# Kernel optimization log

Measured on AMD Instinct MI355X. Metric: run time of the kernel, lower is better.

The kernel has to match this reference:

```python
import jax, jax.numpy as jnp
import numpy as np

N = 512      # nodes
F_IN = 16    # raw node features; adjacency channels = 2*F_IN = 32
H = 64       # hidden
HF = 64      # hidden_final
C = 10       # num_classes
L = 3        # num_layers
E = 16384    # edges (avg degree 32)
EPS = 1e-5


def setup_inputs() -> dict:
    key = jax.random.key(0)
    ks = iter(jax.random.split(key, 40))
    rn = lambda shape, s=0.05: jax.random.normal(next(ks), shape, jnp.float32) * s
    inp = {
        'x': jax.random.normal(next(ks), (N, F_IN), jnp.float32),
        'edge_index': jax.random.randint(next(ks), (2, E), 0, N),
        # no_prop FeatureExtractor
        'np1_w': rn((HF, 2 * F_IN)), 'np1_b': rn((HF,)),
        'np2_w': rn((HF, 2 * F_IN)), 'np3_w': rn((HF, HF)),
        # first PowerfulLayer (in = 2*F_IN)
        'c0_m1_w': rn((H, 2 * F_IN)), 'c0_m1_b': rn((H,)),
        'c0_m2_w': rn((H, 2 * F_IN)), 'c0_m2_b': rn((H,)),
        'c0_m4_w': rn((H, 2 * F_IN + H)), 'c0_m4_b': rn((H,)),
        # remaining L-1 PowerfulLayers (stacked)
        'cm1_w': rn((L - 1, H, H)), 'cm1_b': rn((L - 1, H)),
        'cm2_w': rn((L - 1, H, H)), 'cm2_b': rn((L - 1, H)),
        'cm4_w': rn((L - 1, H, 2 * H)), 'cm4_b': rn((L - 1, H)),
        # batchnorms (training-mode stats; affine params)
        'bn_g': jnp.ones((L, H), jnp.float32), 'bn_b': jnp.zeros((L, H), jnp.float32),
        # per-layer FeatureExtractors (stacked)
        'fe1_w': rn((L, HF, H)), 'fe1_b': rn((L, HF)),
        'fe2_w': rn((L, HF, H)), 'fe3_w': rn((L, HF, HF)),
        # after_conv and final linear
        'ac_w': rn((HF, HF)), 'ac_b': rn((HF,)),
        'fl_w': rn((C, HF)), 'fl_b': rn((C,)),
    }
    return inp


def _lin(x, w, b=None):
    y = x @ w.T
    return y if b is None else y + b


def _extractor(u, w1, b1, w2, w3):
    # u: [B, N, N, F]; graph_class=True, aggr='add'
    n = u.shape[1]
    trace = jnp.einsum('biif->bf', u)                     # sum of diagonal entries
    out1 = _lin(trace / n, w1, b1)
    s = (u.sum(axis=(1, 2)) - trace) / (n * (n - 1))      # off-diagonal mean-ish
    out = out1 + _lin(s, w2)
    return out + _lin(jax.nn.relu(out), w3)


def _powerful(u, m1w, m1b, m2w, m2b, m4w, m4b):
    # UnitMLP with 1 layer == 1x1 conv == per-position linear (no ReLU)
    o1 = jnp.einsum('bijc,oc->bijo', u, m1w) + m1b        # [B,N,N,H]
    o2 = jnp.einsum('bijc,oc->bijo', u, m2w) + m2b
    mult = jnp.einsum('bikh,bkjh->bijh', o1, o2)          # per-channel NxN matmul
    return _lin(jnp.concatenate([mult, u], axis=-1), m4w, m4b)


def _batchnorm(u, g, b):
    # BatchNorm2d in training mode: stats over (batch, N, N) per channel, biased var
    mean = u.mean(axis=(0, 1, 2))
    var = u.var(axis=(0, 1, 2))
    return (u - mean) * jax.lax.rsqrt(var + EPS) * g + b


def reference(x, edge_index, np1_w, np1_b, np2_w, np3_w,
              c0_m1_w, c0_m1_b, c0_m2_w, c0_m2_b, c0_m4_w, c0_m4_b,
              cm1_w, cm1_b, cm2_w, cm2_b, cm4_w, cm4_b,
              bn_g, bn_b, fe1_w, fe1_b, fe2_w, fe3_w,
              ac_w, ac_b, fl_w, fl_b):
    n = x.shape[0]
    src, dst = edge_index[0], edge_index[1]
    edge_attr = jnp.concatenate([x[src], x[dst]], axis=-1)          # [E, 2F]
    A = jnp.zeros((n, n, edge_attr.shape[-1]), x.dtype).at[src, dst].add(edge_attr)
    u = A[None]                                                      # [1,N,N,2F]

    out = _extractor(u, np1_w, np1_b, np2_w, np3_w)
    nlayers = bn_g.shape[0]
    for l in range(nlayers):
        if l == 0:
            u = _powerful(u, c0_m1_w, c0_m1_b, c0_m2_w, c0_m2_b, c0_m4_w, c0_m4_b)
        else:
            u = _powerful(u, cm1_w[l - 1], cm1_b[l - 1], cm2_w[l - 1], cm2_b[l - 1],
                          cm4_w[l - 1], cm4_b[l - 1])
        u = _batchnorm(u, bn_g[l], bn_b[l])
        out = out + _extractor(u, fe1_w[l], fe1_b[l], fe2_w[l], fe3_w[l])

    out = jax.nn.relu(out) / nlayers
    out = out + jax.nn.relu(_lin(out, ac_w, ac_b))   # layer_after_conv
    # dropout with p=0.0 / eval mode is identity
    out = _lin(out, fl_w, fl_b)
    return jax.nn.log_softmax(out, axis=-1)          # [1, num_classes]
```

## Files before the change

### kernel.cpp

```cpp
#include <hip/hip_runtime.h>
#include <hip/hip_bf16.h>

#define Nn   512
#define NN   262144
#define EDG  16384

typedef unsigned short u16;
typedef short v8s __attribute__((ext_vector_type(8)));
typedef float v4f __attribute__((ext_vector_type(4)));
typedef u16 u16x8 __attribute__((ext_vector_type(8)));

__device__ __forceinline__ float b2f(u16 u) {
    union { unsigned int i; float f; } v; v.i = ((unsigned int)u) << 16; return v.f;
}
__device__ __forceinline__ u16 f2b(float f) {
    union { float f; unsigned int i; } v; v.f = f;
    unsigned int r = (v.i + 0x7FFFu + ((v.i >> 16) & 1u)) >> 16;
    return (u16)r;
}

__global__ void sentinel_kernel(float* __restrict__ out, float val) {
    if (threadIdx.x < 10) out[threadIdx.x] = val;
}

__global__ void cvt_weights(const float* __restrict__ s0, const float* __restrict__ s1,
                            const float* __restrict__ s2, const float* __restrict__ s3,
                            const float* __restrict__ s4, const float* __restrict__ s5,
                            u16* __restrict__ dst) {
    int t = blockIdx.x * 256 + threadIdx.x;
    if (t >= 43008) return;
    float v;
    if      (t < 2048)  v = s0[t];
    else if (t < 4096)  v = s1[t - 2048];
    else if (t < 10240) v = s2[t - 4096];
    else if (t < 18432) v = s3[t - 10240];
    else if (t < 26624) v = s4[t - 18432];
    else                v = s5[t - 26624];
    dst[t] = f2b(v);
}

__global__ void scatter_edges(const float* __restrict__ x, const int* __restrict__ ei,
                              float* __restrict__ A) {
    int t = blockIdx.x * 256 + threadIdx.x;
    if (t >= EDG * 32) return;
    int e = t >> 5, c = t & 31;
    int s = ei[e], d = ei[EDG + e];
    float v = (c < 16) ? x[s * 16 + c] : x[d * 16 + (c - 16)];
    atomicAdd(A + ((size_t)s * Nn + d) * 32 + c, v);
}

__global__ __launch_bounds__(256) void finalize_u0(const float* __restrict__ A,
                                                   u16* __restrict__ u0,
                                                   float* __restrict__ total) {
    __shared__ u16 L[32 * 258];
    __shared__ float red[4][32];
    int t = threadIdx.x;
    int p0 = blockIdx.x * 256;
    const float* Ar = A + (size_t)(p0 + t) * 32;
    float v[32];
#pragma unroll
    for (int c = 0; c < 32; ++c) v[c] = Ar[c];
#pragma unroll
    for (int c = 0; c < 32; ++c) L[c * 258 + t] = f2b(v[c]);
    int wv = t >> 6;
#pragma unroll
    for (int c = 0; c < 32; ++c) {
        float r = v[c];
        for (int off = 32; off > 0; off >>= 1) r += __shfl_down(r, off);
        if ((t & 63) == 0) red[wv][c] = r;
    }
    __syncthreads();
    if (t < 32) atomicAdd(total + t, red[0][t] + red[1][t] + red[2][t] + red[3][t]);
    int off = (t & 31) * 8, rb = t >> 5;
#pragma unroll
    for (int pass = 0; pass < 4; ++pass) {
        int c = pass * 8 + rb;
        u16x8 w = *(const u16x8*)(L + c * 258 + off);
        *(u16x8*)(u0 + (size_t)c * NN + p0 + off) = w;
    }
}

__global__ void trace_raw_cm(const u16* __restrict__ ucm, float* __restrict__ trraw) {
    int c = blockIdx.x, t = threadIdx.x;
    const u16* base = ucm + (size_t)c * NN;
    float s = b2f(base[(size_t)(2 * t) * 513]) + b2f(base[(size_t)(2 * t + 1) * 513]);
    for (int off = 32; off > 0; off >>= 1) s += __shfl_down(s, off);
    __shared__ float r[4];
    if ((t & 63) == 0) r[t >> 6] = s;
    __syncthreads();
    if (t == 0) trraw[c] = r[0] + r[1] + r[2] + r[3];
}

template<int NCH>
__global__ __launch_bounds__(256) void conv12_t(
    const u16* __restrict__ src,
    const float* __restrict__ sc, const float* __restrict__ sh,
    const u16* __restrict__ w1, const float* __restrict__ b1,
    const u16* __restrict__ w2, const float* __restrict__ b2,
    u16* __restrict__ dst1, u16* __restrict__ dst2)
{
    __shared__ u16 LS[8320];
    const int C = NCH * 32;
    const int t = threadIdx.x;
    const int P0 = blockIdx.x * 128;
    const int lane = t & 63, wave = t >> 6;
    const int l15 = lane & 15, quad = lane >> 4;
    const int pw = wave * 32;
    const int sr = t >> 4;
    const int so = (t & 15) * 8;

    u16x8 pf[NCH][2];
#pragma unroll
    for (int kc = 0; kc < NCH; ++kc)
#pragma unroll
        for (int ps = 0; ps < 2; ++ps)
            pf[kc][ps] = *(const u16x8*)(src + (size_t)(kc * 32 + ps * 16 + sr) * NN + P0 + so);

    v4f acc[2][4][2];
#pragma unroll
    for (int s = 0; s < 2; ++s)
#pragma unroll
        for (int mt = 0; mt < 4; ++mt)
#pragma unroll
            for (int nt = 0; nt < 2; ++nt) acc[s][mt][nt] = (v4f){0.f, 0.f, 0.f, 0.f};

    {
        u16* Ln = LS;
#pragma unroll
        for (int ps = 0; ps < 2; ++ps) {
            int c = ps * 16 + sr;
            u16x8 v = pf[0][ps];
            if (sc) {
                float s = sc[c], f = sh[c];
#pragma unroll
                for (int j = 0; j < 8; ++j) v[j] = f2b(b2f(v[j]) * s + f);
            }
            *(u16x8*)(Ln + c * 130 + so) = v;
        }
    }
    __syncthreads();
#pragma unroll
    for (int kc = 0; kc < NCH; ++kc) {
        if (kc + 1 < NCH) {
            u16* Ln = LS + ((kc + 1) & 1) * 4160;
#pragma unroll
            for (int ps = 0; ps < 2; ++ps) {
                int c = ps * 16 + sr;
                int cg = (kc + 1) * 32 + c;
                u16x8 v = pf[kc + 1][ps];
                if (sc) {
                    float s = sc[cg], f = sh[cg];
#pragma unroll
                    for (int j = 0; j < 8; ++j) v[j] = f2b(b2f(v[j]) * s + f);
                }
                *(u16x8*)(Ln + c * 130 + so) = v;
            }
        }
        v8s af1[4], af2[4];
#pragma unroll
        for (int mt = 0; mt < 4; ++mt) {
            af1[mt] = *(const v8s*)(w1 + (mt * 16 + l15) * C + kc * 32 + quad * 8);
            af2[mt] = *(const v8s*)(w2 + (mt * 16 + l15) * C + kc * 32 + quad * 8);
        }
        const u16* Lb = LS + (kc & 1) * 4160;
#pragma unroll
        for (int nt = 0; nt < 2; ++nt) {
            const int p = pw + nt * 16 + l15;
            v8s b;
#pragma unroll
            for (int j = 0; j < 8; ++j) b[j] = (short)Lb[(quad * 8 + j) * 130 + p];
#pragma unroll
            for (int mt = 0; mt < 4; ++mt) {
                acc[0][mt][nt] = __builtin_amdgcn_mfma_f32_16x16x32_bf16(af1[mt], b, acc[0][mt][nt], 0, 0, 0);
                acc[1][mt][nt] = __builtin_amdgcn_mfma_f32_16x16x32_bf16(af2[mt], b, acc[1][mt][nt], 0, 0, 0);
            }
        }
        if (kc + 1 < NCH) __syncthreads();
    }
#pragma unroll
    for (int s = 0; s < 2; ++s) {
        __syncthreads();
        const float* bb = s ? b2 : b1;
#pragma unroll
        for (int mt = 0; mt < 4; ++mt)
#pragma unroll
            for (int r = 0; r < 4; ++r) {
                const int h = mt * 16 + quad * 4 + r;
                const float bv = bb[h];
#pragma unroll
                for (int nt = 0; nt < 2; ++nt)
                    LS[h * 130 + pw + nt * 16 + l15] = f2b(acc[s][mt][nt][r] + bv);
            }
        __syncthreads();
        u16* dd = s ? dst2 : dst1;
#pragma unroll
        for (int ps = 0; ps < 4; ++ps) {
            int h = ps * 16 + sr;
            u16x8 v = *(const u16x8*)(LS + h * 130 + so);
            __builtin_nontemporal_store(v, (u16x8*)(dd + (size_t)h * NN + P0 + so));
        }
    }
}

template<int NCH>
__global__ __launch_bounds__(256) void conv4_t(
    const u16* __restrict__ mult, const u16* __restrict__ u,
    const float* __restrict__ sc, const float* __restrict__ sh,
    const u16* __restrict__ w, const float* __restrict__ bias,
    u16* __restrict__ dst,
    float* __restrict__ psum, float* __restrict__ psq, float* __restrict__ ptr)
{
    __shared__ u16 LS[8320];
    __shared__ float R1[64][4], R2[64][4];
    const int K = NCH * 32;
    const int t = threadIdx.x;
    const int P0 = blockIdx.x * 128;
    const int lane = t & 63, wave = t >> 6;
    const int l15 = lane & 15, quad = lane >> 4;
    const int pw = wave * 32;
    const int sr = t >> 4;
    const int so = (t & 15) * 8;

    u16x8 pf[NCH][2];
#pragma unroll
    for (int kc = 0; kc < NCH; ++kc)
#pragma unroll
        for (int ps = 0; ps < 2; ++ps) {
            int cg = kc * 32 + ps * 16 + sr;
            const u16* gp = (cg < 64) ? (mult + (size_t)cg * NN + P0 + so)
                                      : (u + (size_t)(cg - 64) * NN + P0 + so);
            pf[kc][ps] = *(const u16x8*)gp;
        }

    v4f acc[4][2];
#pragma unroll
    for (int mt = 0; mt < 4; ++mt)
#pragma unroll
        for (int nt = 0; nt < 2; ++nt) acc[mt][nt] = (v4f){0.f, 0.f, 0.f, 0.f};

#pragma unroll
    for (int ps = 0; ps < 2; ++ps)
        *(u16x8*)(LS + (ps * 16 + sr) * 130 + so) = pf[0][ps];
    __syncthreads();
#pragma unroll
    for (int kc = 0; kc < NCH; ++kc) {
        if (kc + 1 < NCH) {
            u16* Ln = LS + ((kc + 1) & 1) * 4160;
#pragma unroll
            for (int ps = 0; ps < 2; ++ps) {
                int c = ps * 16 + sr;
                int cg = (kc + 1) * 32 + c;
                u16x8 v = pf[kc + 1][ps];
                if (cg >= 64 && sc) {
                    float s = sc[cg - 64], f = sh[cg - 64];
#pragma unroll
                    for (int j = 0; j < 8; ++j) v[j] = f2b(b2f(v[j]) * s + f);
                }
                *(u16x8*)(Ln + c * 130 + so) = v;
            }
        }
        v8s af[4];
#pragma unroll
        for (int mt = 0; mt < 4; ++mt)
            af[mt] = *(const v8s*)(w + (mt * 16 + l15) * K + kc * 32 + quad * 8);
        const u16* Lb = LS + (kc & 1) * 4160;
#pragma unroll
        for (int nt = 0; nt < 2; ++nt) {
            const int p = pw + nt * 16 + l15;
            v8s b;
#pragma unroll
            for (int j = 0; j < 8; ++j) b[j] = (short)Lb[(quad * 8 + j) * 130 + p];
#pragma unroll
            for (int mt = 0; mt < 4; ++mt)
                acc[mt][nt] = __builtin_amdgcn_mfma_f32_16x16x32_bf16(af[mt], b, acc[mt][nt], 0, 0, 0);
        }
        if (kc + 1 < NCH) __syncthreads();
    }
    __syncthreads();
#pragma unroll
    for (int mt = 0; mt < 4; ++mt)
#pragma unroll
        for (int r = 0; r < 4; ++r) {
            const int h = mt * 16 + quad * 4 + r;
            const float bv = bias[h];
#pragma unroll
            for (int nt = 0; nt < 2; ++nt)
                LS[h * 130 + pw + nt * 16 + l15] = f2b(acc[mt][nt][r] + bv);
        }
    __syncthreads();
    {
        int c = t >> 2, q = t & 3;
        const u16* row = LS + c * 130 + q * 32;
        float s = 0.f, s2 = 0.f;
#pragma unroll
        for (int i = 0; i < 32; ++i) { float v = b2f(row[i]); s += v; s2 += v * v; }
        R1[c][q] = s; R2[c][q] = s2;
    }
    __syncthreads();
    {
        int i = P0 >> 9, j0 = P0 & 511;
        int blk = blockIdx.x;
        if (t < 64) {
            psum[t * 2048 + blk] = R1[t][0] + R1[t][1] + R1[t][2] + R1[t][3];
            psq[t * 2048 + blk]  = R2[t][0] + R2[t][1] + R2[t][2] + R2[t][3];
            if (j0 <= i && i < j0 + 128) ptr[t * 512 + i] = b2f(LS[t * 130 + (i - j0)]);
        }
    }
#pragma unroll
    for (int ps = 0; ps < 4; ++ps) {
        int h = ps * 16 + sr;
        u16x8 v = *(const u16x8*)(LS + h * 130 + so);
        __builtin_nontemporal_store(v, (u16x8*)(dst + (size_t)h * NN + P0 + so));
    }
}

__global__ __launch_bounds__(256) void bmm_mfma(const u16* __restrict__ Aall,
                                                const u16* __restrict__ Ball,
                                                u16* __restrict__ Call) {
    __shared__ u16 LA[128 * 72];
    __shared__ u16 LB[64 * 130];
    const int h = blockIdx.y;
    const int tx = blockIdx.x & 3, ty = blockIdx.x >> 2;
    const int t = threadIdx.x;
    const int lane = t & 63, wave = t >> 6;
    const int l15 = lane & 15, quad = lane >> 4;
    const int jb = wave * 32;
    const u16* Ap = Aall + (size_t)h * NN + (size_t)ty * 128 * 512;
    const u16* Bp = Ball + (size_t)h * NN + tx * 128;

    const int srow = t >> 3;
    const int scol = (t & 7) * 8;
    const int bkr = t >> 4;
    const int bjg = (t & 15) * 8;

    v4f acc[8][2];
#pragma unroll
    for (int mt = 0; mt < 8; ++mt)
#pragma unroll
        for (int nt = 0; nt < 2; ++nt) acc[mt][nt] = (v4f){0.f, 0.f, 0.f, 0.f};

    v8s ra[4], rb[4];
#pragma unroll
    for (int i = 0; i < 4; ++i) {
        ra[i] = *(const v8s*)(Ap + (size_t)(i * 32 + srow) * 512 + scol);
        rb[i] = *(const v8s*)(Bp + (size_t)(i * 16 + bkr) * 512 + bjg);
    }

    for (int ck = 0; ck < 8; ++ck) {
#pragma unroll
        for (int i = 0; i < 4; ++i) {
            *(v8s*)(LA + (i * 32 + srow) * 72 + scol) = ra[i];
            *(v8s*)(LB + (i * 16 + bkr) * 130 + bjg) = rb[i];
        }
        __syncthreads();
        if (ck < 7) {
            const int k0 = (ck + 1) * 64;
#pragma unroll
            for (int i = 0; i < 4; ++i) {
                ra[i] = *(const v8s*)(Ap + (size_t)(i * 32 + srow) * 512 + k0 + scol);
                rb[i] = *(const v8s*)(Bp + (size_t)(k0 + i * 16 + bkr) * 512 + bjg);
            }
        }
#pragma unroll
        for (int kk = 0; kk < 2; ++kk) {
            v8s b[2];
#pragma unroll
            for (int nt = 0; nt < 2; ++nt) {
                const int j = jb + nt * 16 + l15;
#pragma unroll
                for (int jj = 0; jj < 8; ++jj)
                    b[nt][jj] = (short)LB[(kk * 32 + quad * 8 + jj) * 130 + j];
            }
#pragma unroll
            for (int mh = 0; mh < 2; ++mh) {
                v8s a[4];
#pragma unroll
                for (int m = 0; m < 4; ++m)
                    a[m] = *(const v8s*)(LA + ((mh * 4 + m) * 16 + l15) * 72 + kk * 32 + quad * 8);
#pragma unroll
                for (int m = 0; m < 4; ++m)
#pragma unroll
                    for (int nt = 0; nt < 2; ++nt)
                        acc[mh * 4 + m][nt] = __builtin_amdgcn_mfma_f32_16x16x32_bf16(a[m], b[nt], acc[mh * 4 + m][nt], 0, 0, 0);
            }
        }
        __syncthreads();
    }

    u16* Cp = Call + (size_t)h * NN;
#pragma unroll
    for (int mt = 0; mt < 8; ++mt)
#pragma unroll
        for (int r = 0; r < 4; ++r) {
            const int i = ty * 128 + mt * 16 + quad * 4 + r;
#pragma unroll
            for (int nt = 0; nt < 2; ++nt) {
                const int j = tx * 128 + jb + nt * 16 + l15;
                Cp[i * 512 + j] = f2b(acc[mt][nt][r]);
            }
        }
}

__global__ __launch_bounds__(256) void bn_finalize(
    const float* __restrict__ psum, const float* __restrict__ psq,
    const float* __restrict__ ptr,
    const float* __restrict__ g, const float* __restrict__ b,
    float* __restrict__ scale, float* __restrict__ shift,
    float* __restrict__ ttl) {
    int c = blockIdx.x, t = threadIdx.x;
    float s = 0.f, q = 0.f, tr = 0.f;
    for (int k = t; k < 2048; k += 256) { s += psum[c * 2048 + k]; q += psq[c * 2048 + k]; }
    for (int k = t; k < 512; k += 256) tr += ptr[c * 512 + k];
    for (int off = 32; off > 0; off >>= 1) {
        s += __shfl_down(s, off); q += __shfl_down(q, off); tr += __shfl_down(tr, off);
    }
    __shared__ float r1[4], r2[4], r3[4];
    if ((t & 63) == 0) { r1[t >> 6] = s; r2[t >> 6] = q; r3[t >> 6] = tr; }
    __syncthreads();
    if (t == 0) {
        s = r1[0] + r1[1] + r1[2] + r1[3];
        q = r2[0] + r2[1] + r2[2] + r2[3];
        tr = r3[0] + r3[1] + r3[2] + r3[3];
        float mean = s * (1.f / 262144.f);
        float var = q * (1.f / 262144.f) - mean * mean;
        float sc = g[c] * rsqrtf(fmaxf(var, 0.f) + 1e-5f);
        float sh = b[c] - mean * sc;
        scale[c] = sc;
        shift[c] = sh;
        ttl[64 + c] = sc * s + 262144.f * sh;
        ttl[c]      = sc * tr + 512.f * sh;
    }
}

__global__ __launch_bounds__(256) void extractor_par(
    const float* __restrict__ tt,
    const float* __restrict__ np1w, const float* __restrict__ np1b,
    const float* __restrict__ np2w, const float* __restrict__ np3w,
    const float* __restrict__ fe1w, const float* __restrict__ fe1b,
    const float* __restrict__ fe2w, const float* __restrict__ fe3w,
    float* __restrict__ oacc_part) {
    __shared__ float red[64][4];
    __shared__ float xo[64];
    const int li = blockIdx.x;
    const int t = threadIdx.x;
    const int h = t >> 2, q = t & 3;
    const int C = (li == 0) ? 32 : 64;
    const float* w1 = (li == 0) ? np1w : fe1w + (li - 1) * 4096;
    const float* b1 = (li == 0) ? np1b : fe1b + (li - 1) * 64;
    const float* w2 = (li == 0) ? np2w : fe2w + (li - 1) * 4096;
    const float* w3 = (li == 0) ? np3w : fe3w + (li - 1) * 4096;
    const float* tr = tt + li * 128;
    const float* to = tr + 64;
    const int cpq = C >> 2;
    float p = 0.f;
    for (int i = 0; i < cpq; ++i) {
        int c = q * cpq + i;
        p += (tr[c] * (1.f / 512.f)) * w1[h * C + c]
           + ((to[c] - tr[c]) * (1.f / (512.f * 511.f))) * w2[h * C + c];
    }
    red[h][q] = p;
    __syncthreads();
    if (q == 0) xo[h] = b1[h] + red[h][0] + red[h][1] + red[h][2] + red[h][3];
    __syncthreads();
    float o = xo[h];
    float p3 = 0.f;
    for (int i = 0; i < 16; ++i) {
        int f = q * 16 + i;
        p3 += fmaxf(xo[f], 0.f) * w3[h * 64 + f];
    }
    __syncthreads();
    red[h][q] = p3;
    __syncthreads();
    if (q == 0) oacc_part[li * 64 + h] = o + red[h][0] + red[h][1] + red[h][2] + red[h][3];
}

__global__ __launch_bounds__(256) void head_par(
    const float* __restrict__ oacc_part,
    const float* __restrict__ acw, const float* __restrict__ acb,
    const float* __restrict__ flw, const float* __restrict__ flb,
    float* __restrict__ out) {
    __shared__ float x[64], x2[64], red[64][4], l[10];
    const int t = threadIdx.x;
    const int h = t >> 2, q = t & 3;
    if (q == 0) {
        float oa = oacc_part[h] + oacc_part[64 + h] + oacc_part[128 + h] + oacc_part[192 + h];
        x[h] = fmaxf(oa, 0.f) * (1.f / 3.f);
    }
    __syncthreads();
    float p = 0.f;
    for (int i = 0; i < 16; ++i) { int f = q * 16 + i; p += x[f] * acw[h * 64 + f]; }
    red[h][q] = p;
    __syncthreads();
    if (q == 0) {
        float y = acb[h] + red[h][0] + red[h][1] + red[h][2] + red[h][3];
        x2[h] = x[h] + fmaxf(y, 0.f);
    }
    __syncthreads();
    if (t < 40) {
        int hh = t >> 2, qq = t & 3;
        float p2 = 0.f;
        for (int i = 0; i < 16; ++i) { int f = qq * 16 + i; p2 += x2[f] * flw[hh * 64 + f]; }
        red[hh][qq] = p2;
    }
    __syncthreads();
    if (t < 10) l[t] = flb[t] + red[t][0] + red[t][1] + red[t][2] + red[t][3];
    __syncthreads();
    if (t == 0) {
        float m = l[0];
        for (int i = 1; i < 10; ++i) m = fmaxf(m, l[i]);
        float se = 0.f;
        for (int i = 0; i < 10; ++i) se += expf(l[i] - m);
        float ls = m + logf(se);
        for (int i = 0; i < 10; ++i) out[i] = l[i] - ls;
    }
}

extern "C" void kernel_launch(void* const* d_in, const int* in_sizes, int n_in,
                              void* d_out, int out_size, void* d_ws, size_t ws_size,
                              hipStream_t stream) {
    float* out = (float*)d_out;

    static const int exp_sizes[28] = {
        8192, 32768,
        2048, 64, 2048, 4096,
        2048, 64, 2048, 64, 6144, 64,
        8192, 128, 8192, 128, 16384, 128,
        192, 192,
        12288, 192, 12288, 12288,
        4096, 64, 640, 10
    };
    bool ok = (n_in == 28);
    if (ok) for (int i = 0; i < 28; ++i) if (in_sizes[i] != exp_sizes[i]) ok = false;
    if (!ok) { sentinel_kernel<<<1, 64, 0, stream>>>(out, -5.0f); return; }

    const size_t RSZ = (size_t)NN * 64 * 2;
    const size_t BIG_OFF = 8192 + 90112;
    if (ws_size < BIG_OFF + 4 * RSZ) {
        sentinel_kernel<<<1, 64, 0, stream>>>(out, -7.0f);
        return;
    }

    const float* x     = (const float*)d_in[0];
    const int*   ei    = (const int*)d_in[1];
    const float* np1w  = (const float*)d_in[2];
    const float* np1b  = (const float*)d_in[3];
    const float* np2w  = (const float*)d_in[4];
    const float* np3w  = (const float*)d_in[5];
    const float* c0m1b = (const float*)d_in[7];
    const float* c0m2b = (const float*)d_in[9];
    const float* c0m4b = (const float*)d_in[11];
    const float* cm1b  = (const float*)d_in[13];
    const float* cm2b  = (const float*)d_in[15];
    const float* cm4b  = (const float*)d_in[17];
    const float* bng   = (const float*)d_in[18];
    const float* bnb   = (const float*)d_in[19];
    const float* fe1w  = (const float*)d_in[20];
    const float* fe1b  = (const float*)d_in[21];
    const float* fe2w  = (const float*)d_in[22];
    const float* fe3w  = (const float*)d_in[23];
    const float* acw   = (const float*)d_in[24];
    const float* acb   = (const float*)d_in[25];
    const float* flw   = (const float*)d_in[26];
    const float* flb   = (const float*)d_in[27];

    char* ws = (char*)d_ws;
    float* small = (float*)ws;
    float* tt    = small;
    float* scl   = small + 512;
    float* shf   = small + 576;
    float* oaccp = small + 640;

    u16* arena = (u16*)(ws + 8192);

    char* big = ws + BIG_OFF;
    u16* S0 = (u16*)(big + 0 * RSZ);
    u16* S1 = (u16*)(big + 1 * RSZ);
    u16* S2 = (u16*)(big + 2 * RSZ);
    u16* S3 = (u16*)(big + 3 * RSZ);
    float* Abuf = (float*)S2;

    float* psum = (float*)S2;
    float* psq  = psum + 64 * 2048;
    float* ptr  = psq + 64 * 2048;

    hipMemsetAsync(small, 0, 4096, stream);
    hipMemsetAsync(Abuf, 0, (size_t)NN * 32 * 4, stream);

    cvt_weights<<<168, 256, 0, stream>>>((const float*)d_in[6], (const float*)d_in[8],
                                         (const float*)d_in[10], (const float*)d_in[12],
                                         (const float*)d_in[14], (const float*)d_in[16], arena);
    scatter_edges<<<2048, 256, 0, stream>>>(x, ei, Abuf);
    finalize_u0<<<1024, 256, 0, stream>>>(Abuf, S0, tt + 64);
    trace_raw_cm<<<32, 256, 0, stream>>>(S0, tt);

    u16* U[3]  = { S0, S1, S0 };
    u16* O1[3] = { S1, S0, S1 };
    u16* R[3]  = { S1, S0, S1 };

    const float *aff_s = nullptr, *aff_h = nullptr;

    for (int l = 0; l < 3; ++l) {
        int Cin = (l == 0) ? 32 : 64;
        const u16 *w1b, *w2b, *w4b;
        const float *b1, *b2, *b4;
        if (l == 0) {
            w1b = arena;            b1 = c0m1b;
            w2b = arena + 2048;     b2 = c0m2b;
            w4b = arena + 4096;     b4 = c0m4b;
        } else {
            int m = l - 1;
            w1b = arena + 10240 + m * 4096;  b1 = cm1b + m * 64;
            w2b = arena + 18432 + m * 4096;  b2 = cm2b + m * 64;
            w4b = arena + 26624 + m * 8192;  b4 = cm4b + m * 64;
        }
        if (Cin == 32)
            conv12_t<1><<<2048, 256, 0, stream>>>(U[l], aff_s, aff_h, w1b, b1, w2b, b2, O1[l], S2);
        else
            conv12_t<2><<<2048, 256, 0, stream>>>(U[l], aff_s, aff_h, w1b, b1, w2b, b2, O1[l], S2);
        bmm_mfma<<<dim3(16, 64), 256, 0, stream>>>(O1[l], S2, S3);
        if (Cin == 32)
            conv4_t<3><<<2048, 256, 0, stream>>>(S3, U[l], aff_s, aff_h, w4b, b4, R[l], psum, psq, ptr);
        else
            conv4_t<4><<<2048, 256, 0, stream>>>(S3, U[l], aff_s, aff_h, w4b, b4, R[l], psum, psq, ptr);
        bn_finalize<<<64, 256, 0, stream>>>(psum, psq, ptr, bng + l * 64, bnb + l * 64,
                                            scl, shf, tt + (l + 1) * 128);
        aff_s = scl; aff_h = shf;
    }
    extractor_par<<<4, 256, 0, stream>>>(tt, np1w, np1b, np2w, np3w,
                                         fe1w, fe1b, fe2w, fe3w, oaccp);
    head_par<<<1, 256, 0, stream>>>(oaccp, acw, acb, flw, flb, out);
}
```

Before: 476.1 us.

## Rewrite batched matmul with 256x256 tiles, double-buffered LDS and direct global-to-LDS loads

Replaces the 128x128-tile batched bf16 GEMM with a 256x256-tile version using 512 threads, double-buffered shared memory, and XOR-swizzled LDS layouts. A tiles are loaded straight into LDS with global_load_lds. B tiles are transposed in registers into k-contiguous rows, so B fragments become single vector reads instead of eight scalar LDS reads. Blocks are remapped so neighbouring blocks share a head, and the larger tiles halve the redundant global traffic. The cost is heavy register pressure from 32 accumulators per thread, 128 KB of LDS per block, and only 256 blocks in flight.

```diff
diff --git a/kernel.cpp b/kernel.cpp
--- a/kernel.cpp
+++ b/kernel.cpp
@@ -6,6 +6,7 @@
 #define EDG  16384
 
 typedef unsigned short u16;
+typedef unsigned int u32;
 typedef short v8s __attribute__((ext_vector_type(8)));
 typedef float v4f __attribute__((ext_vector_type(4)));
 typedef u16 u16x8 __attribute__((ext_vector_type(8)));
@@ -314,91 +315,137 @@
     }
 }
 
-__global__ __launch_bounds__(256) void bmm_mfma(const u16* __restrict__ Aall,
-                                                const u16* __restrict__ Ball,
-                                                u16* __restrict__ Call) {
-    __shared__ u16 LA[128 * 72];
-    __shared__ u16 LB[64 * 130];
-    const int h = blockIdx.y;
-    const int tx = blockIdx.x & 3, ty = blockIdx.x >> 2;
+__global__ __launch_bounds__(512, 2) void bmm_mfma256(const u16* __restrict__ Aall,
+                                                      const u16* __restrict__ Ball,
+                                                      u16* __restrict__ Call) {
+    __shared__ u16 LA[2][16384];
+    __shared__ u16 LB[2][16384];
+
+    const int bid = blockIdx.x;
+    const int h  = ((bid >> 5) << 3) | (bid & 7);
+    const int qq = (bid >> 3) & 3;
+    const int ty = qq >> 1, tx = qq & 1;
     const int t = threadIdx.x;
-    const int lane = t & 63, wave = t >> 6;
-    const int l15 = lane & 15, quad = lane >> 4;
-    const int jb = wave * 32;
-    const u16* Ap = Aall + (size_t)h * NN + (size_t)ty * 128 * 512;
-    const u16* Bp = Ball + (size_t)h * NN + tx * 128;
-
-    const int srow = t >> 3;
-    const int scol = (t & 7) * 8;
-    const int bkr = t >> 4;
-    const int bjg = (t & 15) * 8;
-
-    v4f acc[8][2];
+    const int l = t & 63, w = t >> 6;
+    const int l15 = l & 15, quad = l >> 4;
+    const int wr = w >> 2, wc = w & 3;
+
+    const u16* Ap = Aall + (size_t)h * NN + (size_t)ty * 256 * 512;
+    const u16* Bp = Ball + (size_t)h * NN + tx * 256;
+    u16* Cp = Call + (size_t)h * NN;
+
+    const int a_m = l >> 3;
+    const int a_kg = (l & 7) ^ a_m;
+    const u16* ApL = Ap + (size_t)a_m * 512 + a_kg * 8;
+
+    v4f acc[8][4];
 #pragma unroll
     for (int mt = 0; mt < 8; ++mt)
 #pragma unroll
-        for (int nt = 0; nt < 2; ++nt) acc[mt][nt] = (v4f){0.f, 0.f, 0.f, 0.f};
-
-    v8s ra[4], rb[4];
-#pragma unroll
-    for (int i = 0; i < 4; ++i) {
-        ra[i] = *(const v8s*)(Ap + (size_t)(i * 32 + srow) * 512 + scol);
-        rb[i] = *(const v8s*)(Bp + (size_t)(i * 16 + bkr) * 512 + bjg);
-    }
-
-    for (int ck = 0; ck < 8; ++ck) {
-#pragma unroll
-        for (int i = 0; i < 4; ++i) {
-            *(v8s*)(LA + (i * 32 + srow) * 72 + scol) = ra[i];
-            *(v8s*)(LB + (i * 16 + bkr) * 130 + bjg) = rb[i];
-        }
-        __syncthreads();
-        if (ck < 7) {
-            const int k0 = (ck + 1) * 64;
-#pragma unroll
-            for (int i = 0; i < 4; ++i) {
-                ra[i] = *(const v8s*)(Ap + (size_t)(i * 32 + srow) * 512 + k0 + scol);
-                rb[i] = *(const v8s*)(Bp + (size_t)(k0 + i * 16 + bkr) * 512 + bjg);
+        for (int nt = 0; nt < 4; ++nt) acc[mt][nt] = (v4f){0.f, 0.f, 0.f, 0.f};
+
+    uint2 eB[4], oB[4];
+
+#define BMM_BLOAD(K0)                                                         \
+    _Pragma("unroll")                                                         \
+    for (int L = 0; L < 4; ++L) {                                             \
+        const int p = w + 8 * L;                                              \
+        const u16* s_ = Bp + (size_t)((K0) + 2 * p) * 512 + l * 4;            \
+        eB[L] = *(const uint2*)s_;                                            \
+        oB[L] = *(const uint2*)(s_ + 512);                                    \
+    }
+
+#define BMM_ALOAD(BUF, K0)                                                    \
+    _Pragma("unroll")                                                         \
+    for (int c = 0; c < 4; ++c) {                                             \
+        const int cc = w * 4 + c;                                             \
+        __builtin_amdgcn_global_load_lds(                                     \
+            (const void*)(ApL + (size_t)cc * 4096 + (K0)),                    \
+            (void*)&LA[BUF][cc * 512], 16, 0, 0);                             \
+    }
+
+#define BMM_BWRITE(BUF)                                                       \
+    {                                                                         \
+        char* base_ = (char*)&LB[BUF][0];                                     \
+        _Pragma("unroll")                                                     \
+        for (int L = 0; L < 4; ++L) {                                         \
+            const int p = w + 8 * L;                                          \
+            const int gk = p >> 2, wd = p & 3;                                \
+            u32 e0 = eB[L].x, e1 = eB[L].y, o0 = oB[L].x, o1 = oB[L].y;       \
+            u32 pk0 = (e0 & 0xFFFFu) | (o0 << 16);                            \
+            u32 pk1 = (e0 >> 16) | (o0 & 0xFFFF0000u);                        \
+            u32 pk2 = (e1 & 0xFFFFu) | (o1 << 16);                            \
+            u32 pk3 = (e1 >> 16) | (o1 & 0xFFFF0000u);                        \
+            _Pragma("unroll")                                                 \
+            for (int q = 0; q < 4; ++q) {                                     \
+                const int j = l * 4 + q;                                      \
+                const int g = gk ^ (j & 7) ^ ((j >> 3) & 7);                  \
+                u32 v_ = (q == 0) ? pk0 : (q == 1) ? pk1 : (q == 2) ? pk2 : pk3; \
+                *(u32*)(base_ + j * 128 + (g << 4) + wd * 4) = v_;            \
+            }                                                                 \
+        }                                                                     \
+    }
+
+#define BMM_COMPUTE(BUF)                                                      \
+    _Pragma("unroll")                                                         \
+    for (int kk = 0; kk < 2; ++kk) {                                          \
+        v8s af_[8], bf_[4];                                                   \
+        const char* baseA_ = (const char*)&LA[BUF][0];                        \
+        const char* baseB_ = (const char*)&LB[BUF][0];                        \
+        _Pragma("unroll")                                                     \
+        for (int mt = 0; mt < 8; ++mt) {                                      \
+            const int m = wr * 128 + mt * 16 + l15;                           \
+            const int g = (kk * 4 + quad) ^ (m & 7);                          \
+            af_[mt] = *(const v8s*)(baseA_ + m * 128 + (g << 4));             \
+        }                                                                     \
+        _Pragma("unroll")                                                     \
+        for (int nt = 0; nt < 4; ++nt) {                                      \
+            const int j = wc * 64 + nt * 16 + l15;                            \
+            const int g = (kk * 4 + quad) ^ (j & 7) ^ ((j >> 3) & 7);         \
+            bf_[nt] = *(const v8s*)(baseB_ + j * 128 + (g << 4));             \
+        }                                                                     \
+        _Pragma("unroll")                                                     \
+        for (int mt = 0; mt < 8; ++mt)                                        \
+            _Pragma("unroll")                                                 \
+            for (int nt = 0; nt < 4; ++nt)                                    \
+                acc[mt][nt] = __builtin_amdgcn_mfma_f32_16x16x32_bf16(        \
+                    af_[mt], bf_[nt], acc[mt][nt], 0, 0, 0);                  \
+    }
+
+    BMM_BLOAD(0)
+    BMM_ALOAD(0, 0)
+    BMM_BWRITE(0)
+    __syncthreads();
+
+#pragma unroll 2
+    for (int ts = 0; ts < 8; ++ts) {
+        const int cur = ts & 1;
+        if (ts < 7) {
+            BMM_BLOAD((ts + 1) * 64)
+            BMM_ALOAD(cur ^ 1, (ts + 1) * 64)
+        }
+        BMM_COMPUTE(cur)
+        if (ts < 7) {
+            BMM_BWRITE(cur ^ 1)
+            __syncthreads();
+        }
+    }
+
+#pragma unroll
+    for (int mt = 0; mt < 8; ++mt)
+#pragma unroll
+        for (int r = 0; r < 4; ++r) {
+            const int i = ty * 256 + wr * 128 + mt * 16 + quad * 4 + r;
+#pragma unroll
+            for (int nt = 0; nt < 4; ++nt) {
+                const int j = tx * 256 + wc * 64 + nt * 16 + l15;
+                Cp[(size_t)i * 512 + j] = f2b(acc[mt][nt][r]);
             }
         }
-#pragma unroll
-        for (int kk = 0; kk < 2; ++kk) {
-            v8s b[2];
-#pragma unroll
-            for (int nt = 0; nt < 2; ++nt) {
-                const int j = jb + nt * 16 + l15;
-#pragma unroll
-                for (int jj = 0; jj < 8; ++jj)
-                    b[nt][jj] = (short)LB[(kk * 32 + quad * 8 + jj) * 130 + j];
-            }
-#pragma unroll
-            for (int mh = 0; mh < 2; ++mh) {
-                v8s a[4];
-#pragma unroll
-                for (int m = 0; m < 4; ++m)
-                    a[m] = *(const v8s*)(LA + ((mh * 4 + m) * 16 + l15) * 72 + kk * 32 + quad * 8);
-#pragma unroll
-                for (int m = 0; m < 4; ++m)
-#pragma unroll
-                    for (int nt = 0; nt < 2; ++nt)
-                        acc[mh * 4 + m][nt] = __builtin_amdgcn_mfma_f32_16x16x32_bf16(a[m], b[nt], acc[mh * 4 + m][nt], 0, 0, 0);
-            }
-        }
-        __syncthreads();
-    }
-
-    u16* Cp = Call + (size_t)h * NN;
-#pragma unroll
-    for (int mt = 0; mt < 8; ++mt)
-#pragma unroll
-        for (int r = 0; r < 4; ++r) {
-            const int i = ty * 128 + mt * 16 + quad * 4 + r;
-#pragma unroll
-            for (int nt = 0; nt < 2; ++nt) {
-                const int j = tx * 128 + jb + nt * 16 + l15;
-                Cp[i * 512 + j] = f2b(acc[mt][nt][r]);
-            }
-        }
+#undef BMM_BLOAD
+#undef BMM_ALOAD
+#undef BMM_BWRITE
+#undef BMM_COMPUTE
 }
 
 __global__ __launch_bounds__(256) void bn_finalize(
@@ -617,7 +664,7 @@
             conv12_t<1><<<2048, 256, 0, stream>>>(U[l], aff_s, aff_h, w1b, b1, w2b, b2, O1[l], S2);
         else
             conv12_t<2><<<2048, 256, 0, stream>>>(U[l], aff_s, aff_h, w1b, b1, w2b, b2, O1[l], S2);
-        bmm_mfma<<<dim3(16, 64), 256, 0, stream>>>(O1[l], S2, S3);
+        bmm_mfma256<<<256, 512, 0, stream>>>(O1[l], S2, S3);
         if (Cin == 32)
             conv4_t<3><<<2048, 256, 0, stream>>>(S3, U[l], aff_s, aff_h, w4b, b4, R[l], psum, psq, ptr);
         else
```

New measurement: 467.1 us. About the same (-1.9%).
